# Kernel tuning notes

Measured on AMD Instinct MI355X. Metric: run time of the kernel, lower is better.

The kernel has to match this reference:

```python
import jax, jax.numpy as jnp
import numpy as np
from jax import lax

CH = 16      # channel_n
HID = 128    # hidden_n
WDIM = 128   # w_dim


def _sobel_weight():
    sx = np.array([[-1, 0, 1], [-2, 0, 2], [-1, 0, 1]], dtype=np.float32).reshape(1, 1, 3, 3)
    sy = np.array([[-1, -2, -1], [0, 0, 0], [1, 2, 1]], dtype=np.float32).reshape(1, 1, 3, 3)
    sx = np.repeat(sx, CH, axis=0)  # [16,1,3,3]
    sy = np.repeat(sy, CH, axis=0)  # [16,1,3,3]
    return jnp.asarray(np.concatenate([sx, sy], axis=0))  # [32,1,3,3] torch grouped-conv OIHW layout


def setup_inputs() -> dict:
    key = jax.random.key(0)
    k1, k2, k3, k4 = jax.random.split(key, 4)
    B, H, W = 8, 96, 96
    x = jax.random.uniform(k1, (B, CH, H, W), dtype=jnp.float32)
    w = jax.random.normal(k2, (B, WDIM), dtype=jnp.float32)
    sobel = _sobel_weight()
    # update_net params. NOTE: original fills W2 with 0.0 (trivial delta); we use
    W1 = jax.random.normal(k3, (HID, 3 * CH + WDIM), dtype=jnp.float32) * 0.05
    b1 = jnp.zeros((HID,), dtype=jnp.float32)
    W2 = jax.random.normal(k4, (CH, HID), dtype=jnp.float32) * 0.02
    return {"x": x, "w": w, "sobel": sobel, "W1": W1, "b1": b1, "W2": W2, "steps": 64}


def _living_mask(alpha):
    # max_pool2d(3, stride=1, pad=1) > 0.1 ; torch pads with -inf for max pool
    m = lax.reduce_window(alpha, -jnp.inf, lax.max, (1, 1, 3, 3), (1, 1, 1, 1), 'SAME')
    return m > 0.1


def reference(x, w, sobel, W1, b1, W2, steps):
    B, _, H, Wd = x.shape
    w_exp = jnp.broadcast_to(w[:, :, None, None], (B, WDIM, H, Wd))

    def step(xc, key):
        pre_life = _living_mask(xc[:, 3:4])
        perception = lax.conv_general_dilated(
            xc, sobel, (1, 1), 'SAME', feature_group_count=CH,
            dimension_numbers=('NCHW', 'OIHW', 'NCHW'))  # [B,32,H,W]
        comb = jnp.concatenate([xc, perception, w_exp], axis=1)  # [B,176,H,W]
        h = jax.nn.relu(jnp.einsum('bchw,nc->bnhw', comb, W1) + b1[None, :, None, None])
        delta = jnp.einsum('bnhw,cn->bchw', h, W2)
        alpha = xc[:, 3:4]
        upd = (jax.random.uniform(key, alpha.shape) < 0.5) & (alpha > 0.1)
        xn = xc + delta * upd.astype(xc.dtype)
        life = pre_life & _living_mask(xn[:, 3:4])
        xn = xn * life.astype(xn.dtype)
        return xn, None

    keys = jax.random.split(jax.random.key(42), steps)
    x_final, _ = lax.scan(step, x, keys)
    return x_final
```

## Files before the change

kernel.cpp:

```cpp
#include <hip/hip_runtime.h>
#include <stdint.h>


#define CHN 16
#define HIDN 128
#define WD 128
#define NB 8
#define NH 96
#define NW 96
#define NSTEPS 64
#define TW 16
#define TH 4
#define PLANE (NH*NW)
#define TILES_X (NW/TW)
#define TILES_Y (NH/TH)
#define TPI (TILES_X*TILES_Y)
#define NBLK (NB*TPI)
#define HW_ (TH+2)
#define WW_ (TW+2)
#define NF4 (HW_*WW_*4)
#define NT 256

typedef float v2f __attribute__((ext_vector_type(2)));

__host__ __device__ __forceinline__ uint32_t rotl(uint32_t v, int d){ return (v<<d)|(v>>(32-d)); }

__host__ __device__ __forceinline__ void threefry2x32(uint32_t k0, uint32_t k1,
                                                      uint32_t x0, uint32_t x1,
                                                      uint32_t &o0, uint32_t &o1){
  uint32_t k2 = k0 ^ k1 ^ 0x1BD11BDAu;
  x0 += k0; x1 += k1;
  x0 += x1; x1 = rotl(x1,13); x1 ^= x0;
  x0 += x1; x1 = rotl(x1,15); x1 ^= x0;
  x0 += x1; x1 = rotl(x1,26); x1 ^= x0;
  x0 += x1; x1 = rotl(x1, 6); x1 ^= x0;
  x0 += k1; x1 += k2 + 1u;
  x0 += x1; x1 = rotl(x1,17); x1 ^= x0;
  x0 += x1; x1 = rotl(x1,29); x1 ^= x0;
  x0 += x1; x1 = rotl(x1,16); x1 ^= x0;
  x0 += x1; x1 = rotl(x1,24); x1 ^= x0;
  x0 += k2; x1 += k0 + 2u;
  x0 += x1; x1 = rotl(x1,13); x1 ^= x0;
  x0 += x1; x1 = rotl(x1,15); x1 ^= x0;
  x0 += x1; x1 = rotl(x1,26); x1 ^= x0;
  x0 += x1; x1 = rotl(x1, 6); x1 ^= x0;
  x0 += k0; x1 += k1 + 3u;
  x0 += x1; x1 = rotl(x1,17); x1 ^= x0;
  x0 += x1; x1 = rotl(x1,29); x1 ^= x0;
  x0 += x1; x1 = rotl(x1,16); x1 ^= x0;
  x0 += x1; x1 = rotl(x1,24); x1 ^= x0;
  x0 += k1; x1 += k2 + 4u;
  x0 += x1; x1 = rotl(x1,13); x1 ^= x0;
  x0 += x1; x1 = rotl(x1,15); x1 ^= x0;
  x0 += x1; x1 = rotl(x1,26); x1 ^= x0;
  x0 += x1; x1 = rotl(x1, 6); x1 ^= x0;
  x0 += k2; x1 += k0 + 5u;
  o0 = x0; o1 = x1;
}

__global__ __launch_bounds__(256) void nca_pre(
    const float* __restrict__ w, const float* __restrict__ W1,
    const float* __restrict__ b1, const float* __restrict__ W2,
    float* __restrict__ w1eff, float* __restrict__ w2t, float* __restrict__ c1)
{
  const int b = blockIdx.x, t = threadIdx.x;
  if (b == 0){
    for (int idx = t; idx < HIDN*32; idx += 256){
      int n = idx >> 5, k = idx & 31;
      float v;
      if (k < 16) v = W1[n*176 + k];
      else { int cc = k - 16; v = W1[n*176 + 16 + 2*cc] + W1[n*176 + 17 + 2*cc]; }
      w1eff[idx] = v;
    }
    for (int idx = t; idx < HIDN*CHN; idx += 256){
      int n = idx >> 4, cc = idx & 15;
      w2t[idx] = W2[cc*HIDN + n];
    }
  }
  if (t < HIDN){
    float s = b1[t];
    const float* wrow = W1 + t*176 + 48;
    const float* wb = w + b*WD;
    #pragma unroll 8
    for (int k = 0; k < WD; ++k) s = fmaf(wrow[k], wb[k], s);
    c1[b*HIDN + t] = s;
  }
}

template<bool FIRST>
__global__ __launch_bounds__(NT, 4) void nca_step(
    const float* __restrict__ Xin,
    const unsigned char* __restrict__ Mp,
    const float* __restrict__ w1eff, const float* __restrict__ w2t,
    const float* __restrict__ c1,
    uint32_t key0, uint32_t key1,
    float* __restrict__ Yn, unsigned char* __restrict__ Mn)
{
  __shared__ __align__(16) float w1s[HIDN*32];
  __shared__ float xs[HW_][WW_][20];
  __shared__ float ya[TH+4][TW+4];
  __shared__ float lifes[HW_][WW_];
  __shared__ float ufs[64];
  __shared__ float red2[2][CHN][64];

  const int T = blockIdx.x;
  const int b = T & 7;
  const int t = T >> 3;
  const int tw0 = (t % TILES_X)*TW, th0 = (t / TILES_X)*TH;
  const int tid = threadIdx.x;

  {
    const float4* src = (const float4*)w1eff;
    float4* dst = (float4*)w1s;
    #pragma unroll
    for (int i = 0; i < 4; ++i) dst[tid + i*NT] = src[tid + i*NT];
  }

  if (FIRST){
    for (int idx = tid; idx < CHN*HW_*WW_; idx += NT){
      int ch = idx / (HW_*WW_), rem = idx % (HW_*WW_);
      int hh = rem / WW_, ww = rem % WW_;
      int g2 = th0 - 1 + hh, w2 = tw0 - 1 + ww;
      float v = 0.f;
      if ((unsigned)g2 < NH && (unsigned)w2 < NW)
        v = Xin[((b*CHN + ch)*NH + g2)*NW + w2];
      xs[hh][ww][ch] = v;
    }
  } else {
    if (tid < (TH+4)*(TW+4)){
      int hh = tid / (TW+4), ww = tid % (TW+4);
      int g2 = th0 - 2 + hh, w2 = tw0 - 2 + ww;
      float v = 0.f;
      if ((unsigned)g2 < NH && (unsigned)w2 < NW)
        v = Xin[(size_t)(b*PLANE + g2*NW + w2)*CHN + 3];
      ya[hh][ww] = v;
    }
    float4 xr[2];
    #pragma unroll
    for (int i = 0; i < 2; ++i){
      int idx = tid + i*NT;
      float4 v = make_float4(0.f,0.f,0.f,0.f);
      if (idx < NF4){
        int hh = idx / (WW_*4);
        int rem = idx % (WW_*4);
        int ww = rem >> 2, k4 = rem & 3;
        int g2 = th0 - 1 + hh, w2 = tw0 - 1 + ww;
        if ((unsigned)g2 < NH && (unsigned)w2 < NW)
          v = *(const float4*)(Xin + (size_t)(b*PLANE + g2*NW + w2)*CHN + k4*4);
      }
      xr[i] = v;
    }
    __syncthreads();
    if (tid < HW_*WW_){
      int hh = tid / WW_, ww = tid % WW_;
      int g2 = th0 - 1 + hh, w2 = tw0 - 1 + ww;
      float lf = 0.f;
      if ((unsigned)g2 < NH && (unsigned)w2 < NW){
        float mx = ya[hh][ww];
        #pragma unroll
        for (int dr = 0; dr < 3; ++dr)
          #pragma unroll
          for (int dc = 0; dc < 3; ++dc)
            mx = fmaxf(mx, ya[hh+dr][ww+dc]);
        lf = (Mp[b*PLANE + g2*NW + w2] && (mx > 0.1f)) ? 1.f : 0.f;
      }
      lifes[hh][ww] = lf;
    }
    __syncthreads();
    #pragma unroll
    for (int i = 0; i < 2; ++i){
      int idx = tid + i*NT;
      if (idx < NF4){
        int hh = idx / (WW_*4);
        int rem = idx % (WW_*4);
        int ww = rem >> 2, k4 = rem & 3;
        float lf = lifes[hh][ww];
        float4 v = xr[i];
        v.x *= lf; v.y *= lf; v.z *= lf; v.w *= lf;
        *(float4*)&xs[hh][ww][k4*4] = v;
      }
    }
  }
  __syncthreads();

  const int px = tid & 63;
  const int q  = tid >> 6;
  const int c = px & 15, r = px >> 4;
  const int gh = th0 + r, gw = tw0 + c;
  const int pos = b*PLANE + gh*NW + gw;

  #define LD4(dr,dc,k4) (*(const float4*)&xs[r+(dr)][c+(dc)][(k4)*4])
  const v2f two = (v2f){2.f, 2.f};
  float4 xc4[4];
  v2f xp[8], pp[8];
  #pragma unroll
  for (int k4 = 0; k4 < 4; ++k4){
    xc4[k4] = LD4(1,1,k4);
    xp[2*k4]   = (v2f){xc4[k4].x, xc4[k4].y};
    xp[2*k4+1] = (v2f){xc4[k4].z, xc4[k4].w};
  }
  #pragma unroll
  for (int k4 = 0; k4 < 2; ++k4){
    float4 a = LD4(0,2,k4), b0 = LD4(0,0,k4);
    float4 d = LD4(1,2,k4), e = LD4(1,0,k4);
    float4 f = LD4(2,2,k4), g = LD4(2,0,k4);
    v2f a0 = (v2f){a.x,a.y}, a1 = (v2f){a.z,a.w};
    v2f b0v= (v2f){b0.x,b0.y},b1v= (v2f){b0.z,b0.w};
    v2f d0 = (v2f){d.x,d.y}, d1 = (v2f){d.z,d.w};
    v2f e0 = (v2f){e.x,e.y}, e1 = (v2f){e.z,e.w};
    v2f f0 = (v2f){f.x,f.y}, f1 = (v2f){f.z,f.w};
    v2f g0 = (v2f){g.x,g.y}, g1 = (v2f){g.z,g.w};
    pp[2*k4]   = (a0-b0v) + two*(d0-e0) + (f0-g0);
    pp[2*k4+1] = (a1-b1v) + two*(d1-e1) + (f1-g1);
  }
  #pragma unroll
  for (int k4 = 2; k4 < 4; ++k4){
    float4 a = LD4(2,0,k4), b0 = LD4(0,0,k4);
    float4 d = LD4(2,1,k4), e = LD4(0,1,k4);
    float4 f = LD4(2,2,k4), g = LD4(0,2,k4);
    v2f a0 = (v2f){a.x,a.y}, a1 = (v2f){a.z,a.w};
    v2f b0v= (v2f){b0.x,b0.y},b1v= (v2f){b0.z,b0.w};
    v2f d0 = (v2f){d.x,d.y}, d1 = (v2f){d.z,d.w};
    v2f e0 = (v2f){e.x,e.y}, e1 = (v2f){e.z,e.w};
    v2f f0 = (v2f){f.x,f.y}, f1 = (v2f){f.z,f.w};
    v2f g0 = (v2f){g.x,g.y}, g1 = (v2f){g.z,g.w};
    pp[2*k4]   = (a0-b0v) + two*(d0-e0) + (f0-g0);
    pp[2*k4+1] = (a1-b1v) + two*(d1-e1) + (f1-g1);
  }
  #undef LD4

  if (q == 0){
    uint32_t o0, o1;
    threefry2x32(key0, key1, 0u, (uint32_t)pos, o0, o1);
    ufs[px] = ((((o0 ^ o1) >> 31) == 0u) && (xc4[0].w > 0.1f)) ? 1.f : 0.f;
  } else if (q == 1){
    float mx = xs[r][c][3];
    #pragma unroll
    for (int dr = 0; dr < 3; ++dr)
      #pragma unroll
      for (int dc = 0; dc < 3; ++dc)
        mx = fmaxf(mx, xs[r+dr][c+dc][3]);
    Mn[pos] = (mx > 0.1f) ? (unsigned char)1 : (unsigned char)0;
  }

  v2f acc2[8];
  #pragma unroll
  for (int i = 0; i < 8; ++i) acc2[i] = (v2f){0.f, 0.f};
  const int nbase = __builtin_amdgcn_readfirstlane(q) << 5;
  const float* c1b = c1 + b*HIDN;

  #pragma unroll 2
  for (int nn = 0; nn < 32; ++nn){
    const int n = nbase + nn;
    const v2f* wx = (const v2f*)(w1s + (n << 5));
    v2f h01 = (v2f){c1b[n], 0.f};
    v2f h23 = (v2f){0.f, 0.f};
    #pragma unroll
    for (int k = 0; k < 8; ++k){
      h01 = __builtin_elementwise_fma(xp[k], wx[k],   h01);
      h23 = __builtin_elementwise_fma(pp[k], wx[8+k], h23);
    }
    float hv = fmaxf((h01.x + h01.y) + (h23.x + h23.y), 0.f);
    v2f hvv = (v2f){hv, hv};
    const v2f* w2p = (const v2f*)(w2t + (n << 4));
    #pragma unroll
    for (int cc2 = 0; cc2 < 8; ++cc2)
      acc2[cc2] = __builtin_elementwise_fma(hvv, w2p[cc2], acc2[cc2]);
  }

  if (q >= 2){
    #pragma unroll
    for (int cc2 = 0; cc2 < 8; ++cc2){
      red2[q-2][2*cc2  ][px] = acc2[cc2].x;
      red2[q-2][2*cc2+1][px] = acc2[cc2].y;
    }
  }
  __syncthreads();
  if (q < 2){
    #pragma unroll
    for (int cc2 = 0; cc2 < 8; ++cc2){
      acc2[cc2].x += red2[q][2*cc2  ][px];
      acc2[cc2].y += red2[q][2*cc2+1][px];
    }
    #pragma unroll
    for (int cc2 = 0; cc2 < 8; ++cc2){
      red2[q][2*cc2  ][px] = acc2[cc2].x;
      red2[q][2*cc2+1][px] = acc2[cc2].y;
    }
  }
  __syncthreads();

  {
    float uf = ufs[px];
    int ch = q << 2;
    float v0 = red2[0][ch+0][px] + red2[1][ch+0][px];
    float v1 = red2[0][ch+1][px] + red2[1][ch+1][px];
    float v2 = red2[0][ch+2][px] + red2[1][ch+2][px];
    float v3 = red2[0][ch+3][px] + red2[1][ch+3][px];
    float4 o = make_float4(fmaf(v0, uf, xc4[q].x), fmaf(v1, uf, xc4[q].y),
                           fmaf(v2, uf, xc4[q].z), fmaf(v3, uf, xc4[q].w));
    *(float4*)(Yn + (size_t)pos*CHN + q*4) = o;
  }
}

__global__ __launch_bounds__(256) void nca_final(
    const float* __restrict__ Yp, const unsigned char* __restrict__ Mp,
    float* __restrict__ out)
{
  __shared__ float ya[TH+4][TW+4];
  __shared__ float lifes[TH][TW];
  const int T = blockIdx.x;
  const int b = T & 7;
  const int t = T >> 3;
  const int tw0 = (t % TILES_X)*TW, th0 = (t / TILES_X)*TH;
  const int tid = threadIdx.x;
  if (tid < (TH+4)*(TW+4)){
    int hh = tid / (TW+4), ww = tid % (TW+4);
    int g2 = th0 - 2 + hh, w2 = tw0 - 2 + ww;
    float v = 0.f;
    if ((unsigned)g2 < NH && (unsigned)w2 < NW)
      v = Yp[(size_t)(b*PLANE + g2*NW + w2)*CHN + 3];
    ya[hh][ww] = v;
  }
  __syncthreads();
  if (tid < TH*TW){
    int i = tid >> 4, j = tid & 15;
    float mx = ya[i+2][j+2];
    #pragma unroll
    for (int dr = 0; dr < 3; ++dr)
      #pragma unroll
      for (int dc = 0; dc < 3; ++dc)
        mx = fmaxf(mx, ya[i+1+dr][j+1+dc]);
    lifes[i][j] = (Mp[b*PLANE + (th0+i)*NW + (tw0+j)] && (mx > 0.1f)) ? 1.f : 0.f;
  }
  __syncthreads();
  for (int idx = tid; idx < CHN*TH*TW; idx += 256){
    int ch = idx >> 6, p = idx & 63;
    int i = p >> 4, j = p & 15;
    int pos = b*PLANE + (th0+i)*NW + (tw0+j);
    out[((b*CHN + ch)*NH + th0 + i)*NW + tw0 + j] = Yp[(size_t)pos*CHN + ch] * lifes[i][j];
  }
}

extern "C" void kernel_launch(void* const* d_in, const int* in_sizes, int n_in,
                              void* d_out, int out_size, void* d_ws, size_t ws_size,
                              hipStream_t stream) {
  const float* x  = (const float*)d_in[0];
  const float* w  = (const float*)d_in[1];
  const float* W1 = (const float*)d_in[3];
  const float* b1 = (const float*)d_in[4];
  const float* W2 = (const float*)d_in[5];
  float* out = (float*)d_out;
  char* ws = (char*)d_ws;

  size_t off = 0;
  float*    w1eff = (float*)(ws + off);    off += (size_t)HIDN*32*4;
  float*    w2t   = (float*)(ws + off);    off += (size_t)HIDN*CHN*4;
  float*    c1    = (float*)(ws + off);    off += (size_t)NB*HIDN*4;
  float*    Yb0   = (float*)(ws + off);    off += (size_t)NB*CHN*PLANE*4;
  float*    Yb1   = (float*)(ws + off);    off += (size_t)NB*CHN*PLANE*4;
  unsigned char* Mb0 = (unsigned char*)(ws + off); off += (size_t)NB*PLANE;
  unsigned char* Mb1 = (unsigned char*)(ws + off); off += (size_t)NB*PLANE;
  (void)ws_size; (void)in_sizes; (void)n_in; (void)out_size;

  uint32_t k0[NSTEPS], k1[NSTEPS];
  for (int s = 0; s < NSTEPS; ++s) threefry2x32(0u, 42u, 0u, (uint32_t)s, k0[s], k1[s]);

  nca_pre<<<dim3(NB), dim3(256), 0, stream>>>(w, W1, b1, W2, w1eff, w2t, c1);

  nca_step<true><<<dim3(NBLK), dim3(NT), 0, stream>>>(
      x, Mb1 , w1eff, w2t, c1, k0[0], k1[0], Yb0, Mb0);
  for (int s = 1; s < NSTEPS; ++s){
    const float* Yp = (s & 1) ? Yb0 : Yb1;
    float*       Yn = (s & 1) ? Yb1 : Yb0;
    const unsigned char* Mq = (s & 1) ? Mb0 : Mb1;
    unsigned char*       Mn = (s & 1) ? Mb1 : Mb0;
    nca_step<false><<<dim3(NBLK), dim3(NT), 0, stream>>>(
        Yp, Mq, w1eff, w2t, c1, k0[s], k1[s], Yn, Mn);
  }
  nca_final<<<dim3(NBLK), dim3(256), 0, stream>>>(Yb1, Mb1, out);
}
```

Before: 1.366 ms.

## Alias reduction buffer onto tile LDS and raise occupancy target to five blocks

```diff
diff --git a/kernel.cpp b/kernel.cpp
--- a/kernel.cpp
+++ b/kernel.cpp
@@ -88,7 +88,7 @@
 }
 
 template<bool FIRST>
-__global__ __launch_bounds__(NT, 4) void nca_step(
+__global__ __launch_bounds__(NT, 5) void nca_step(
     const float* __restrict__ Xin,
     const unsigned char* __restrict__ Mp,
     const float* __restrict__ w1eff, const float* __restrict__ w2t,
@@ -97,11 +97,13 @@
     float* __restrict__ Yn, unsigned char* __restrict__ Mn)
 {
   __shared__ __align__(16) float w1s[HIDN*32];
-  __shared__ float xs[HW_][WW_][20];
+  __shared__ __align__(16) float xs[HW_][WW_][20];
   __shared__ float ya[TH+4][TW+4];
   __shared__ float lifes[HW_][WW_];
   __shared__ float ufs[64];
-  __shared__ float red2[2][CHN][64];
+
+  float* red2p = &xs[0][0][0];
+  #define RED2(bk,ch,p) red2p[((((bk)<<4)+(ch))<<6)+(p)]
 
   const int T = blockIdx.x;
   const int b = T & 7;
@@ -243,10 +245,16 @@
     Mn[pos] = (mx > 0.1f) ? (unsigned char)1 : (unsigned char)0;
   }
 
+  const int qq = __builtin_amdgcn_readfirstlane(q);
+  float4 myx = xc4[0];
+  if (qq == 1) myx = xc4[1];
+  else if (qq == 2) myx = xc4[2];
+  else if (qq == 3) myx = xc4[3];
+
   v2f acc2[8];
   #pragma unroll
   for (int i = 0; i < 8; ++i) acc2[i] = (v2f){0.f, 0.f};
-  const int nbase = __builtin_amdgcn_readfirstlane(q) << 5;
+  const int nbase = qq << 5;
   const float* c1b = c1 + b*HIDN;
 
   #pragma unroll 2
@@ -268,24 +276,26 @@
       acc2[cc2] = __builtin_elementwise_fma(hvv, w2p[cc2], acc2[cc2]);
   }
 
+  __syncthreads();
+
   if (q >= 2){
     #pragma unroll
     for (int cc2 = 0; cc2 < 8; ++cc2){
-      red2[q-2][2*cc2  ][px] = acc2[cc2].x;
-      red2[q-2][2*cc2+1][px] = acc2[cc2].y;
+      RED2(q-2, 2*cc2  , px) = acc2[cc2].x;
+      RED2(q-2, 2*cc2+1, px) = acc2[cc2].y;
     }
   }
   __syncthreads();
   if (q < 2){
     #pragma unroll
     for (int cc2 = 0; cc2 < 8; ++cc2){
-      acc2[cc2].x += red2[q][2*cc2  ][px];
-      acc2[cc2].y += red2[q][2*cc2+1][px];
+      acc2[cc2].x += RED2(q, 2*cc2  , px);
+      acc2[cc2].y += RED2(q, 2*cc2+1, px);
     }
     #pragma unroll
     for (int cc2 = 0; cc2 < 8; ++cc2){
-      red2[q][2*cc2  ][px] = acc2[cc2].x;
-      red2[q][2*cc2+1][px] = acc2[cc2].y;
+      RED2(q, 2*cc2  , px) = acc2[cc2].x;
+      RED2(q, 2*cc2+1, px) = acc2[cc2].y;
     }
   }
   __syncthreads();
@@ -293,14 +303,15 @@
   {
     float uf = ufs[px];
     int ch = q << 2;
-    float v0 = red2[0][ch+0][px] + red2[1][ch+0][px];
-    float v1 = red2[0][ch+1][px] + red2[1][ch+1][px];
-    float v2 = red2[0][ch+2][px] + red2[1][ch+2][px];
-    float v3 = red2[0][ch+3][px] + red2[1][ch+3][px];
-    float4 o = make_float4(fmaf(v0, uf, xc4[q].x), fmaf(v1, uf, xc4[q].y),
-                           fmaf(v2, uf, xc4[q].z), fmaf(v3, uf, xc4[q].w));
+    float v0 = RED2(0, ch+0, px) + RED2(1, ch+0, px);
+    float v1 = RED2(0, ch+1, px) + RED2(1, ch+1, px);
+    float v2 = RED2(0, ch+2, px) + RED2(1, ch+2, px);
+    float v3 = RED2(0, ch+3, px) + RED2(1, ch+3, px);
+    float4 o = make_float4(fmaf(v0, uf, myx.x), fmaf(v1, uf, myx.y),
+                           fmaf(v2, uf, myx.z), fmaf(v3, uf, myx.w));
     *(float4*)(Yn + (size_t)pos*CHN + q*4) = o;
   }
+  #undef RED2
 }
 
 __global__ __launch_bounds__(256) void nca_final(
```

Result: slower. 1.737 ms (+27.2%).
